# Optimization experiments

Hardware: AMD Instinct MI355X
Metric: run time of the kernel (lower is better)

## Reference

```python
import jax, jax.numpy as jnp
import numpy as np

B, N, F = 2, 2048, 1024
H = 16
DH = F // H  # features per head = 64
SCALE = 1.0 / np.sqrt(DH)


def setup_inputs() -> dict:
    key = jax.random.key(0)
    ks = jax.random.split(key, 11)
    s = 0.02
    return {
        "q": jax.random.normal(ks[0], (B, N, F), dtype=jnp.float32),
        "k": jax.random.normal(ks[1], (B, N, F), dtype=jnp.float32),
        "v": jax.random.normal(ks[2], (B, N, F), dtype=jnp.float32),
        "Wq": jax.random.normal(ks[3], (F, F), dtype=jnp.float32) * s,
        "bq": jnp.zeros((F,), dtype=jnp.float32),
        "Wk": jax.random.normal(ks[4], (F, F), dtype=jnp.float32) * s,
        "bk": jnp.zeros((F,), dtype=jnp.float32),
        "Wv": jax.random.normal(ks[5], (F, F), dtype=jnp.float32) * s,
        "bv": jnp.zeros((F,), dtype=jnp.float32),
        "Wo": jax.random.normal(ks[6], (F, F), dtype=jnp.float32) * s,
        "bo": jnp.zeros((F,), dtype=jnp.float32),
    }


def reference(q, k, v, Wq, bq, Wk, bk, Wv, bv, Wo, bo):
    b = q.shape[0]
    # projections, split into heads: [B, H, N, DH]
    qh = (q @ Wq + bq).reshape(b, -1, H, DH).transpose(0, 2, 1, 3)
    kh = (k @ Wk + bk).reshape(b, -1, H, DH).transpose(0, 2, 1, 3)
    vh = (v @ Wv + bv).reshape(b, -1, H, DH).transpose(0, 2, 1, 3)
    # scaled dot-product attention
    attn = jnp.einsum("bhqd,bhkd->bhqk", qh * SCALE, kh)
    attn = jax.nn.softmax(attn, axis=-1)
    out = jnp.einsum("bhqk,bhkd->bhqd", attn, vh)
    # merge heads: [B, Nq, F]
    out = out.transpose(0, 2, 1, 3).reshape(b, -1, H * DH)
    return out @ Wo + bo
```

## Files before the change

kernel.cpp:

```cpp
#include <hip/hip_runtime.h>
#include <hip/hip_bf16.h>

typedef float f32x4  __attribute__((ext_vector_type(4)));
typedef float f32x16 __attribute__((ext_vector_type(16)));
typedef short s16x8  __attribute__((ext_vector_type(8)));
typedef unsigned int u32;
typedef unsigned short u16;
typedef u16 u16x4 __attribute__((ext_vector_type(4)));
typedef u32 u32x4 __attribute__((ext_vector_type(4)));

#define DEVI static __device__ __forceinline__

constexpr int BB   = 2;
constexpr int SEQ  = 2048;
constexpr int FD   = 1024;
constexpr int NH   = 16;
constexpr int DHD  = 64;
constexpr int MROWS = BB * SEQ;

DEVI u16 f2bf(float x){
  __hip_bfloat16 h = __float2bfloat16(x);
  return __builtin_bit_cast(u16, h);
}
DEVI float bf2f(u16 u){
  return __bfloat162float(__builtin_bit_cast(__hip_bfloat16, u));
}
DEVI u32 pack2(float a, float b){
  return (u32)f2bf(a) | ((u32)f2bf(b) << 16);
}

DEVI void mfma_bf16(f32x4& acc, s16x8 a, s16x8 b){
  asm("v_mfma_f32_16x16x32_bf16 %0, %1, %2, %0" : "+v"(acc) : "v"(a), "v"(b));
}
DEVI void mfma32(f32x16& acc, s16x8 a, s16x8 b){
  asm("v_mfma_f32_32x32x16_bf16 %0, %1, %2, %0" : "+v"(acc) : "v"(a), "v"(b));
}
DEVI void plswap(u32& a, u32& b){
  asm("v_permlane32_swap_b32 %0, %1" : "+v"(a), "+v"(b));
}

#define AS1C(p) ((const __attribute__((address_space(1))) void*)(p))
#define AS3(p)  ((__attribute__((address_space(3))) void*)(p))

__global__ __launch_bounds__(256) void wprep_all(
    const float* __restrict__ W0, const float* __restrict__ W1,
    const float* __restrict__ W2, const float* __restrict__ W3,
    u16* __restrict__ T0, u16* __restrict__ T1,
    u16* __restrict__ T2, u16* __restrict__ T3)
{
  const int z = blockIdx.z;
  const float* W = z==0?W0 : z==1?W1 : z==2?W2 : W3;
  u16* Th       = z==0?T0 : z==1?T1 : z==2?T2 : T3;

  __shared__ float tile[64][65];
  const int kb = blockIdx.x * 64, nb = blockIdx.y * 64;
  const int t  = threadIdx.x;
  const int r  = t >> 2, c0 = (t & 3) * 16;

  const float* src = W + (size_t)(kb + r) * FD + nb + c0;
  #pragma unroll
  for (int i = 0; i < 16; i += 4){
    float4 v = *reinterpret_cast<const float4*>(src + i);
    tile[r][c0+i+0] = v.x; tile[r][c0+i+1] = v.y;
    tile[r][c0+i+2] = v.z; tile[r][c0+i+3] = v.w;
  }
  __syncthreads();

  s16x8 hA, hB;
  #pragma unroll
  for (int i = 0; i < 8; i++){
    hA[i] = (short)f2bf(tile[c0 + i][r]);
    hB[i] = (short)f2bf(tile[c0 + 8 + i][r]);
  }
  const size_t o = (size_t)(nb + r) * FD + kb + c0;
  *reinterpret_cast<s16x8*>(Th + o)     = hA;
  *reinterpret_cast<s16x8*>(Th + o + 8) = hB;
}

__global__ __launch_bounds__(256) void qkv_gemm(
    const float* __restrict__ qp, const float* __restrict__ kp, const float* __restrict__ vp,
    const u16* __restrict__ Wq, const u16* __restrict__ Wk, const u16* __restrict__ Wv,
    const float* __restrict__ bq, const float* __restrict__ bk, const float* __restrict__ bv,
    u16* __restrict__ Q2, u16* __restrict__ K2, u16* __restrict__ Vt2)
{
  constexpr int LDT = 40;
  __shared__ u16 sA[128][LDT];
  __shared__ u16 sW[128][LDT];

  const int z = blockIdx.z;
  const float* Ap   = z==0?qp : z==1?kp : vp;
  const u16*  Wh    = z==0?Wq : z==1?Wk : Wv;
  const float* bias = z==0?bq : z==1?bk : bv;
  u16* outp         = z==0?Q2 : z==1?K2 : Vt2;
  const float oscale = (z==0) ? 0.125f : 1.0f;
  const bool  tr     = (z==2);

  const int t    = threadIdx.x;
  const int nb0  = blockIdx.x * 128, mb0 = blockIdx.y * 128;
  const int lane = t & 63, w = t >> 6;
  const int r16  = lane & 15, g = lane >> 4;
  const int wm   = (w >> 1) * 64, wn = (w & 1) * 64;

  f32x4 acc[4][4] = {};

  for (int kb = 0; kb < FD; kb += 32){
    __syncthreads();
    #pragma unroll
    for (int s = 0; s < 2; s++){
      const int c = t + 256 * s;
      const int row = c >> 2, col = (c & 3) * 8;
      *reinterpret_cast<s16x8*>(&sW[row][col]) =
        *reinterpret_cast<const s16x8*>(Wh + (size_t)(nb0 + row) * FD + kb + col);
      const float* af = Ap + (size_t)(mb0 + row) * FD + kb + col;
      float4 v0 = *reinterpret_cast<const float4*>(af);
      float4 v1 = *reinterpret_cast<const float4*>(af + 4);
      s16x8 hv;
      hv[0]=(short)f2bf(v0.x); hv[1]=(short)f2bf(v0.y);
      hv[2]=(short)f2bf(v0.z); hv[3]=(short)f2bf(v0.w);
      hv[4]=(short)f2bf(v1.x); hv[5]=(short)f2bf(v1.y);
      hv[6]=(short)f2bf(v1.z); hv[7]=(short)f2bf(v1.w);
      *reinterpret_cast<s16x8*>(&sA[row][col]) = hv;
    }
    __syncthreads();

    s16x8 a[4], bh[4];
    #pragma unroll
    for (int i = 0; i < 4; i++){
      a[i]  = *reinterpret_cast<const s16x8*>(&sA[wm + i*16 + r16][g*8]);
      bh[i] = *reinterpret_cast<const s16x8*>(&sW[wn + i*16 + r16][g*8]);
    }
    #pragma unroll
    for (int i = 0; i < 4; i++)
      #pragma unroll
      for (int j = 0; j < 4; j++)
        mfma_bf16(acc[i][j], a[i], bh[j]);
  }

  #pragma unroll
  for (int i = 0; i < 4; i++){
    #pragma unroll
    for (int j = 0; j < 4; j++){
      const int ccol = nb0 + wn + j*16 + r16;
      const float bv = bias[ccol];
      #pragma unroll
      for (int r = 0; r < 4; r++){
        const int m = mb0 + wm + i*16 + g*4 + r;
        const float v = (acc[i][j][r] + bv) * oscale;
        const int b = m >> 11, n = m & (SEQ - 1);
        const int h = ccol >> 6, d = ccol & 63;
        const size_t idx = tr ? ((size_t)(b*NH + h)*DHD + d)*SEQ + n
                              : ((size_t)(b*NH + h)*SEQ + n)*DHD + d;
        outp[idx] = f2bf(v);
      }
    }
  }
}

template<int BM>
__global__ __launch_bounds__(256) void ogemm_k(
    const u16* __restrict__ Ap, const u16* __restrict__ Wh,
    const float* __restrict__ bias, float* __restrict__ outp)
{
  constexpr int LDT = 40;
  constexpr int AI  = BM / 32;
  __shared__ u16 sA[BM][LDT];
  __shared__ u16 sW[128][LDT];

  const int t    = threadIdx.x;
  const int nb0  = blockIdx.x * 128, mb0 = blockIdx.y * BM;
  const int lane = t & 63, w = t >> 6;
  const int r16  = lane & 15, g = lane >> 4;
  const int wm   = (w >> 1) * (BM/2), wn = (w & 1) * 64;

  f32x4 acc[AI][4] = {};

  for (int kb = 0; kb < FD; kb += 32){
    __syncthreads();
    #pragma unroll
    for (int s = 0; s < 2; s++){
      const int c = t + 256 * s;
      const int row = c >> 2, col = (c & 3) * 8;
      *reinterpret_cast<s16x8*>(&sW[row][col]) =
        *reinterpret_cast<const s16x8*>(Wh + (size_t)(nb0 + row) * FD + kb + col);
    }
    #pragma unroll
    for (int s = 0; s < BM/64; s++){
      const int c = t + 256 * s;
      const int row = c >> 2, col = (c & 3) * 8;
      *reinterpret_cast<s16x8*>(&sA[row][col]) =
        *reinterpret_cast<const s16x8*>(Ap + (size_t)(mb0 + row) * FD + kb + col);
    }
    __syncthreads();

    s16x8 a[AI], bh[4];
    #pragma unroll
    for (int i = 0; i < AI; i++)
      a[i]  = *reinterpret_cast<const s16x8*>(&sA[wm + i*16 + r16][g*8]);
    #pragma unroll
    for (int j = 0; j < 4; j++)
      bh[j] = *reinterpret_cast<const s16x8*>(&sW[wn + j*16 + r16][g*8]);
    #pragma unroll
    for (int i = 0; i < AI; i++)
      #pragma unroll
      for (int j = 0; j < 4; j++)
        mfma_bf16(acc[i][j], a[i], bh[j]);
  }

  #pragma unroll
  for (int i = 0; i < AI; i++){
    #pragma unroll
    for (int j = 0; j < 4; j++){
      const int ccol = nb0 + wn + j*16 + r16;
      const float bv = bias[ccol];
      #pragma unroll
      for (int r = 0; r < 4; r++){
        const int m = mb0 + wm + i*16 + g*4 + r;
        outp[(size_t)m * FD + ccol] = acc[i][j][r] + bv;
      }
    }
  }
}

__global__ __launch_bounds__(512, 4) void attn_k(
    const u16* __restrict__ Q2, const u16* __restrict__ K2, const u16* __restrict__ Vt2,
    u16* __restrict__ AOh)
{
  __shared__ u16 smem[2][2][2][64*64];

  const int bid = blockIdx.x + 16 * blockIdx.y;
  const int qt  = bid >> 5;
  const int bh  = (bid & 7) * 4 + ((bid >> 3) & 3);

  const int t = threadIdx.x, w = t >> 6, lane = t & 63;
  const int grp = w >> 2, gw = w & 3;
  const int l31 = lane & 31, hi = lane >> 5;

  const u16* Kb = K2  + (size_t)bh * SEQ * DHD;
  const u16* Vb = Vt2 + (size_t)bh * DHD * SEQ;

  const int srow8  = lane >> 3;
  const int schunk = ((lane & 7) ^ srow8) * 8;

  const int qrow = qt*128 + gw*32 + l31;
  const u16* Qrow = Q2 + ((size_t)bh * SEQ + qrow) * DHD;
  s16x8 qf[4];
  #pragma unroll
  for (int dk = 0; dk < 4; dk++)
    qf[dk] = *reinterpret_cast<const s16x8*>(Qrow + dk*16 + hi*8);

  f32x16 ot0 = {}, ot1 = {};
  float mrun = -1e30f, lrun = 0.f;

  auto stage_tile = [&](int buf, int kt){
    #pragma unroll
    for (int i = 0; i < 2; i++){
      const int row = gw*16 + i*8 + srow8;
      const u16* kg = Kb + (size_t)(kt*64 + row) * DHD + schunk;
      const u16* vg = Vb + (size_t)row * SEQ + kt*64 + schunk;
      __builtin_amdgcn_global_load_lds(AS1C(kg), AS3(&smem[0][grp][buf][(gw*16 + i*8)*64]), 16, 0, 0);
      __builtin_amdgcn_global_load_lds(AS1C(vg), AS3(&smem[1][grp][buf][(gw*16 + i*8)*64]), 16, 0, 0);
    }
  };
  auto lds16 = [](const u16* base, int row, int colbyte) -> s16x8 {
    int off = (row << 7) + colbyte;
    off ^= (row & 7) << 4;
    return *reinterpret_cast<const s16x8*>(reinterpret_cast<const char*>(base) + off);
  };

  constexpr int NIT = SEQ / 64 / 2;
  stage_tile(0, grp);
  __syncthreads();

  for (int i = 0; i < NIT; i++){
    const int buf = i & 1;
    if (i + 1 < NIT) stage_tile(buf ^ 1, 2*(i+1) + grp);
    const u16* sK = &smem[0][grp][buf][0];
    const u16* sV = &smem[1][grp][buf][0];

    f32x16 st0 = {}, st1 = {};
    __builtin_amdgcn_s_setprio(1);
    #pragma unroll
    for (int dk = 0; dk < 4; dk++){
      s16x8 kf0 = lds16(sK, l31,      dk*32 + hi*16);
      s16x8 kf1 = lds16(sK, 32 + l31, dk*32 + hi*16);
      mfma32(st0, kf0, qf[dk]);
      mfma32(st1, kf1, qf[dk]);
    }
    __builtin_amdgcn_s_setprio(0);

    float mx[8];
    #pragma unroll
    for (int r = 0; r < 8; r++)
      mx[r] = fmaxf(fmaxf(st0[r], st0[r+8]), fmaxf(st1[r], st1[r+8]));
    float pmax = fmaxf(fmaxf(fmaxf(mx[0],mx[1]), fmaxf(mx[2],mx[3])),
                       fmaxf(fmaxf(mx[4],mx[5]), fmaxf(mx[6],mx[7])));
    pmax = fmaxf(pmax, __shfl_xor(pmax, 32, 64));

    if (!__all(pmax <= mrun + 8.f)){
      float mnew = fmaxf(mrun, pmax);
      float alp = __expf(mrun - mnew);
      mrun = mnew;
      lrun *= alp;
      #pragma unroll
      for (int r = 0; r < 16; r++){ ot0[r] *= alp; ot1[r] *= alp; }
    }

    #pragma unroll
    for (int r = 0; r < 16; r++){
      st0[r] = __expf(st0[r] - mrun);
      st1[r] = __expf(st1[r] - mrun);
    }
    float s8[8];
    #pragma unroll
    for (int r = 0; r < 8; r++)
      s8[r] = (st0[r] + st0[r+8]) + (st1[r] + st1[r+8]);
    float psum = ((s8[0]+s8[1])+(s8[2]+s8[3])) + ((s8[4]+s8[5])+(s8[6]+s8[7]));
    psum += __shfl_xor(psum, 32, 64);
    lrun += psum;

    u32 pw[16];
    #pragma unroll
    for (int g2 = 0; g2 < 4; g2++){
      pw[g2*2+0]   = pack2(st0[g2*4+0], st0[g2*4+1]);
      pw[g2*2+1]   = pack2(st0[g2*4+2], st0[g2*4+3]);
      pw[8+g2*2+0] = pack2(st1[g2*4+0], st1[g2*4+1]);
      pw[8+g2*2+1] = pack2(st1[g2*4+2], st1[g2*4+3]);
    }
    s16x8 pb[4];
    #pragma unroll
    for (int ks = 0; ks < 4; ks++){
      const int e = (ks>>1)*8 + (ks&1)*4;
      u32 w0 = pw[e+0], w1 = pw[e+1], w2 = pw[e+2], w3 = pw[e+3];
      plswap(w0, w2);
      plswap(w1, w3);
      u32x4 wv = { w0, w1, w2, w3 };
      pb[ks] = __builtin_bit_cast(s16x8, wv);
    }

    __builtin_amdgcn_s_setprio(1);
    #pragma unroll
    for (int ks = 0; ks < 4; ks++){
      s16x8 vf0 = lds16(sV, l31,      ks*32 + hi*16);
      s16x8 vf1 = lds16(sV, 32 + l31, ks*32 + hi*16);
      mfma32(ot0, vf0, pb[ks]);
      mfma32(ot1, vf1, pb[ks]);
    }
    __builtin_amdgcn_s_setprio(0);

    __syncthreads();
  }

  float* sO = reinterpret_cast<float*>(&smem[0][0][0][0]);
  float* sM = reinterpret_cast<float*>(&smem[0][0][0][0]) + 128*68;
  const int ql = gw*32 + l31;

  if (grp == 1){
    #pragma unroll
    for (int r4 = 0; r4 < 4; r4++){
      const int d0 = r4*8 + hi*4;
      #pragma unroll
      for (int j = 0; j < 4; j++){
        sO[ql*68 + d0 + j]      = ot0[r4*4+j];
        sO[ql*68 + 32 + d0 + j] = ot1[r4*4+j];
      }
    }
    if (hi == 0){ sM[ql*2+0] = mrun; sM[ql*2+1] = lrun; }
  }
  __syncthreads();
  if (grp == 0){
    const float m1 = sM[ql*2+0], l1 = sM[ql*2+1];
    const float M  = fmaxf(mrun, m1);
    const float w0 = __expf(mrun - M), w1e = __expf(m1 - M);
    const float inv = 1.0f / (lrun*w0 + l1*w1e);

    const int b = bh >> 4, h = bh & 15;
    u16* orow = AOh + ((size_t)b*SEQ + qrow) * FD + h*64;
    #pragma unroll
    for (int r4 = 0; r4 < 4; r4++){
      const int d0 = r4*8 + hi*4;
      u16x4 v0, v1;
      #pragma unroll
      for (int j = 0; j < 4; j++){
        v0[j] = f2bf((ot0[r4*4+j]*w0 + sO[ql*68 + d0 + j]*w1e) * inv);
        v1[j] = f2bf((ot1[r4*4+j]*w0 + sO[ql*68 + 32 + d0 + j]*w1e) * inv);
      }
      *reinterpret_cast<u16x4*>(orow + d0)      = v0;
      *reinterpret_cast<u16x4*>(orow + 32 + d0) = v1;
    }
  }
}

extern "C" void kernel_launch(void* const* d_in, const int* in_sizes, int n_in,
                              void* d_out, int out_size, void* d_ws, size_t ws_size,
                              hipStream_t stream)
{
  const float* q  = (const float*)d_in[0];
  const float* k  = (const float*)d_in[1];
  const float* v  = (const float*)d_in[2];
  const float* Wq = (const float*)d_in[3];
  const float* bq = (const float*)d_in[4];
  const float* Wk = (const float*)d_in[5];
  const float* bk = (const float*)d_in[6];
  const float* Wv = (const float*)d_in[7];
  const float* bv = (const float*)d_in[8];
  const float* Wo = (const float*)d_in[9];
  const float* bo = (const float*)d_in[10];
  float* out = (float*)d_out;
  (void)in_sizes; (void)n_in; (void)out_size; (void)ws_size;

  char* ws = (char*)d_ws;
  size_t off = 0;
  auto alloc = [&](size_t bytes) -> char* {
    char* p = ws + off;
    off += (bytes + 255) & ~(size_t)255;
    return p;
  };
  const size_t WB = (size_t)FD * FD * sizeof(u16);
  u16* WqTh = (u16*)alloc(WB);
  u16* WkTh = (u16*)alloc(WB);
  u16* WvTh = (u16*)alloc(WB);
  u16* WoTh = (u16*)alloc(WB);
  const size_t QB = (size_t)BB * NH * SEQ * DHD * sizeof(u16);
  u16* Q2  = (u16*)alloc(QB);
  u16* K2  = (u16*)alloc(QB);
  u16* Vt2 = (u16*)alloc(QB);
  const size_t AB = (size_t)BB * SEQ * FD * sizeof(u16);
  u16* AOh = (u16*)alloc(AB);

  wprep_all<<<dim3(16,16,4), 256, 0, stream>>>(Wq, Wk, Wv, Wo, WqTh, WkTh, WvTh, WoTh);

  qkv_gemm<<<dim3(8,32,3), 256, 0, stream>>>(q, k, v, WqTh, WkTh, WvTh,
                                             bq, bk, bv, Q2, K2, Vt2);

  attn_k<<<dim3(16,32), 512, 0, stream>>>(Q2, K2, Vt2, AOh);

  ogemm_k<64><<<dim3(8,64), 256, 0, stream>>>(AOh, WoTh, bo, out);
}
```

Measured before the change: 153.9 us.

## Double-buffer projection GEMMs with direct global-to-LDS loads and XCD-aware block mapping

Both projection GEMMs now stage tiles into double-buffered LDS with global_load_lds and XOR-swizzled layouts, so the next K-slice loads while MFMAs run on the current one and one barrier per iteration is removed. The QKV GEMM stores raw fp32 activations in LDS and converts to bf16 at fragment-read time, which doubles A-tile LDS traffic. Block IDs are remapped so blocks sharing an M strip land on the same XCD for L2 reuse. s_setprio is raised around MFMAs, and launch bounds now request 3 waves per SIMD.

```diff
diff --git a/kernel.cpp b/kernel.cpp
--- a/kernel.cpp
+++ b/kernel.cpp
@@ -16,7 +16,6 @@
 constexpr int FD   = 1024;
 constexpr int NH   = 16;
 constexpr int DHD  = 64;
-constexpr int MROWS = BB * SEQ;
 
 DEVI u16 f2bf(float x){
   __hip_bfloat16 h = __float2bfloat16(x);
@@ -77,17 +76,21 @@
   *reinterpret_cast<s16x8*>(Th + o + 8) = hB;
 }
 
-__global__ __launch_bounds__(256) void qkv_gemm(
+__global__ __launch_bounds__(256, 3) void qkv_gemm(
     const float* __restrict__ qp, const float* __restrict__ kp, const float* __restrict__ vp,
     const u16* __restrict__ Wq, const u16* __restrict__ Wk, const u16* __restrict__ Wv,
     const float* __restrict__ bq, const float* __restrict__ bk, const float* __restrict__ bv,
     u16* __restrict__ Q2, u16* __restrict__ K2, u16* __restrict__ Vt2)
 {
-  constexpr int LDT = 40;
-  __shared__ u16 sA[128][LDT];
-  __shared__ u16 sW[128][LDT];
-
-  const int z = blockIdx.z;
+  __shared__ float sA[2][128*32];
+  __shared__ u16   sW[2][128*32];
+
+  const int bid  = blockIdx.x;
+  const int xcd  = bid & 7, idx = bid >> 3;
+  const int strip = xcd * 12 + (idx >> 3);
+  const int nb   = idx & 7;
+  const int z    = strip >> 5, my = strip & 31;
+
   const float* Ap   = z==0?qp : z==1?kp : vp;
   const u16*  Wh    = z==0?Wq : z==1?Wk : Wv;
   const float* bias = z==0?bq : z==1?bk : bv;
@@ -96,44 +99,73 @@
   const bool  tr     = (z==2);
 
   const int t    = threadIdx.x;
-  const int nb0  = blockIdx.x * 128, mb0 = blockIdx.y * 128;
+  const int nb0  = nb * 128, mb0 = my * 128;
   const int lane = t & 63, w = t >> 6;
   const int r16  = lane & 15, g = lane >> 4;
   const int wm   = (w >> 1) * 64, wn = (w & 1) * 64;
 
+  const int aRow = lane >> 3, aChunk = (lane & 7) ^ aRow;
+  const int wRow = lane >> 2, wChunk = (lane & 3) ^ (wRow & 3);
+
+  auto stage = [&](int buf, int kb){
+    #pragma unroll
+    for (int i = 0; i < 4; i++){
+      const int row = i*32 + w*8 + aRow;
+      const float* ag = Ap + (size_t)(mb0 + row) * FD + kb + aChunk*4;
+      __builtin_amdgcn_global_load_lds(AS1C(ag), AS3(&sA[buf][(i*32 + w*8)*32]), 16, 0, 0);
+    }
+    #pragma unroll
+    for (int i = 0; i < 2; i++){
+      const int row = i*64 + w*16 + wRow;
+      const u16* wg = Wh + (size_t)(nb0 + row) * FD + kb + wChunk*8;
+      __builtin_amdgcn_global_load_lds(AS1C(wg), AS3(&sW[buf][(i*64 + w*16)*32]), 16, 0, 0);
+    }
+  };
+  auto ldsA = [&](const float* base, int row, int gg) -> s16x8 {
+    const char* p = reinterpret_cast<const char*>(base);
+    const int roff = row << 7, sw = (row & 7) << 4;
+    f32x4 lo = *reinterpret_cast<const f32x4*>(p + (roff + ((gg*32)      ^ sw)));
+    f32x4 hi = *reinterpret_cast<const f32x4*>(p + (roff + ((gg*32 + 16) ^ sw)));
+    s16x8 r;
+    #pragma unroll
+    for (int j = 0; j < 4; j++){
+      r[j]   = (short)f2bf(lo[j]);
+      r[4+j] = (short)f2bf(hi[j]);
+    }
+    return r;
+  };
+  auto ldsW = [&](const u16* base, int row, int gg) -> s16x8 {
+    const char* p = reinterpret_cast<const char*>(base);
+    const int off = (row << 6) + ((gg*16) ^ ((row & 3) << 4));
+    return *reinterpret_cast<const s16x8*>(p + off);
+  };
+
   f32x4 acc[4][4] = {};
 
-  for (int kb = 0; kb < FD; kb += 32){
-    __syncthreads();
-    #pragma unroll
-    for (int s = 0; s < 2; s++){
-      const int c = t + 256 * s;
-      const int row = c >> 2, col = (c & 3) * 8;
-      *reinterpret_cast<s16x8*>(&sW[row][col]) =
-        *reinterpret_cast<const s16x8*>(Wh + (size_t)(nb0 + row) * FD + kb + col);
-      const float* af = Ap + (size_t)(mb0 + row) * FD + kb + col;
-      float4 v0 = *reinterpret_cast<const float4*>(af);
-      float4 v1 = *reinterpret_cast<const float4*>(af + 4);
-      s16x8 hv;
-      hv[0]=(short)f2bf(v0.x); hv[1]=(short)f2bf(v0.y);
-      hv[2]=(short)f2bf(v0.z); hv[3]=(short)f2bf(v0.w);
-      hv[4]=(short)f2bf(v1.x); hv[5]=(short)f2bf(v1.y);
-      hv[6]=(short)f2bf(v1.z); hv[7]=(short)f2bf(v1.w);
-      *reinterpret_cast<s16x8*>(&sA[row][col]) = hv;
-    }
-    __syncthreads();
+  stage(0, 0);
+  __syncthreads();
+
+  for (int it = 0; it < FD/32; it++){
+    const int buf = it & 1;
+    if (it + 1 < FD/32) stage(buf ^ 1, (it + 1) * 32);
 
     s16x8 a[4], bh[4];
     #pragma unroll
-    for (int i = 0; i < 4; i++){
-      a[i]  = *reinterpret_cast<const s16x8*>(&sA[wm + i*16 + r16][g*8]);
-      bh[i] = *reinterpret_cast<const s16x8*>(&sW[wn + i*16 + r16][g*8]);
-    }
+    for (int i = 0; i < 4; i++)
+      a[i]  = ldsA(sA[buf], wm + i*16 + r16, g);
+    #pragma unroll
+    for (int j = 0; j < 4; j++)
+      bh[j] = ldsW(sW[buf], wn + j*16 + r16, g);
+
+    __builtin_amdgcn_s_setprio(1);
     #pragma unroll
     for (int i = 0; i < 4; i++)
       #pragma unroll
       for (int j = 0; j < 4; j++)
         mfma_bf16(acc[i][j], a[i], bh[j]);
+    __builtin_amdgcn_s_setprio(0);
+
+    __syncthreads();
   }
 
   #pragma unroll
@@ -148,66 +180,83 @@
         const float v = (acc[i][j][r] + bv) * oscale;
         const int b = m >> 11, n = m & (SEQ - 1);
         const int h = ccol >> 6, d = ccol & 63;
-        const size_t idx = tr ? ((size_t)(b*NH + h)*DHD + d)*SEQ + n
-                              : ((size_t)(b*NH + h)*SEQ + n)*DHD + d;
-        outp[idx] = f2bf(v);
+        const size_t o = tr ? ((size_t)(b*NH + h)*DHD + d)*SEQ + n
+                            : ((size_t)(b*NH + h)*SEQ + n)*DHD + d;
+        outp[o] = f2bf(v);
       }
     }
   }
 }
 
-template<int BM>
-__global__ __launch_bounds__(256) void ogemm_k(
+__global__ __launch_bounds__(256, 3) void ogemm_k(
     const u16* __restrict__ Ap, const u16* __restrict__ Wh,
     const float* __restrict__ bias, float* __restrict__ outp)
 {
-  constexpr int LDT = 40;
-  constexpr int AI  = BM / 32;
-  __shared__ u16 sA[BM][LDT];
-  __shared__ u16 sW[128][LDT];
+  __shared__ u16 sA[2][64*32];
+  __shared__ u16 sW[2][128*32];
+
+  const int bid  = blockIdx.x;
+  const int xcd  = bid & 7, idx = bid >> 3;
+  const int my   = xcd * 8 + (idx >> 3);
+  const int nb   = idx & 7;
 
   const int t    = threadIdx.x;
-  const int nb0  = blockIdx.x * 128, mb0 = blockIdx.y * BM;
+  const int nb0  = nb * 128, mb0 = my * 64;
   const int lane = t & 63, w = t >> 6;
   const int r16  = lane & 15, g = lane >> 4;
-  const int wm   = (w >> 1) * (BM/2), wn = (w & 1) * 64;
-
-  f32x4 acc[AI][4] = {};
-
-  for (int kb = 0; kb < FD; kb += 32){
-    __syncthreads();
-    #pragma unroll
-    for (int s = 0; s < 2; s++){
-      const int c = t + 256 * s;
-      const int row = c >> 2, col = (c & 3) * 8;
-      *reinterpret_cast<s16x8*>(&sW[row][col]) =
-        *reinterpret_cast<const s16x8*>(Wh + (size_t)(nb0 + row) * FD + kb + col);
-    }
-    #pragma unroll
-    for (int s = 0; s < BM/64; s++){
-      const int c = t + 256 * s;
-      const int row = c >> 2, col = (c & 3) * 8;
-      *reinterpret_cast<s16x8*>(&sA[row][col]) =
-        *reinterpret_cast<const s16x8*>(Ap + (size_t)(mb0 + row) * FD + kb + col);
-    }
-    __syncthreads();
-
-    s16x8 a[AI], bh[4];
-    #pragma unroll
-    for (int i = 0; i < AI; i++)
-      a[i]  = *reinterpret_cast<const s16x8*>(&sA[wm + i*16 + r16][g*8]);
+  const int wm   = (w >> 1) * 32, wn = (w & 1) * 64;
+
+  const int wRow = lane >> 2, wChunk = (lane & 3) ^ (wRow & 3);
+
+  auto stage = [&](int buf, int kb){
+    {
+      const int row = w*16 + wRow;
+      const u16* ag = Ap + (size_t)(mb0 + row) * FD + kb + wChunk*8;
+      __builtin_amdgcn_global_load_lds(AS1C(ag), AS3(&sA[buf][(w*16)*32]), 16, 0, 0);
+    }
+    #pragma unroll
+    for (int i = 0; i < 2; i++){
+      const int row = i*64 + w*16 + wRow;
+      const u16* wg = Wh + (size_t)(nb0 + row) * FD + kb + wChunk*8;
+      __builtin_amdgcn_global_load_lds(AS1C(wg), AS3(&sW[buf][(i*64 + w*16)*32]), 16, 0, 0);
+    }
+  };
+  auto ldsW = [&](const u16* base, int row, int gg) -> s16x8 {
+    const char* p = reinterpret_cast<const char*>(base);
+    const int off = (row << 6) + ((gg*16) ^ ((row & 3) << 4));
+    return *reinterpret_cast<const s16x8*>(p + off);
+  };
+
+  f32x4 acc[2][4] = {};
+
+  stage(0, 0);
+  __syncthreads();
+
+  for (int it = 0; it < FD/32; it++){
+    const int buf = it & 1;
+    if (it + 1 < FD/32) stage(buf ^ 1, (it + 1) * 32);
+
+    s16x8 a[2], bh[4];
+    #pragma unroll
+    for (int i = 0; i < 2; i++)
+      a[i]  = ldsW(sA[buf], wm + i*16 + r16, g);
     #pragma unroll
     for (int j = 0; j < 4; j++)
-      bh[j] = *reinterpret_cast<const s16x8*>(&sW[wn + j*16 + r16][g*8]);
-    #pragma unroll
-    for (int i = 0; i < AI; i++)
+      bh[j] = ldsW(sW[buf], wn + j*16 + r16, g);
+
+    __builtin_amdgcn_s_setprio(1);
+    #pragma unroll
+    for (int i = 0; i < 2; i++)
       #pragma unroll
       for (int j = 0; j < 4; j++)
         mfma_bf16(acc[i][j], a[i], bh[j]);
+    __builtin_amdgcn_s_setprio(0);
+
+    __syncthreads();
   }
 
   #pragma unroll
-  for (int i = 0; i < AI; i++){
+  for (int i = 0; i < 2; i++){
     #pragma unroll
     for (int j = 0; j < 4; j++){
       const int ccol = nb0 + wn + j*16 + r16;
@@ -429,10 +478,10 @@
 
   wprep_all<<<dim3(16,16,4), 256, 0, stream>>>(Wq, Wk, Wv, Wo, WqTh, WkTh, WvTh, WoTh);
 
-  qkv_gemm<<<dim3(8,32,3), 256, 0, stream>>>(q, k, v, WqTh, WkTh, WvTh,
-                                             bq, bk, bv, Q2, K2, Vt2);
+  qkv_gemm<<<dim3(768), 256, 0, stream>>>(q, k, v, WqTh, WkTh, WvTh,
+                                          bq, bk, bv, Q2, K2, Vt2);
 
   attn_k<<<dim3(16,32), 512, 0, stream>>>(Q2, K2, Vt2, AOh);
 
-  ogemm_k<64><<<dim3(8,64), 256, 0, stream>>>(AOh, WoTh, bo, out);
-}
+  ogemm_k<<<dim3(512), 256, 0, stream>>>(AOh, WoTh, bo, out);
+}
```

Result: faster. 138.5 us (-10.0%).
